# Optimization experiments

Hardware: AMD Instinct MI355X
Metric: run time of the kernel (lower is better)

Reference implementation:

```python
import jax, jax.numpy as jnp
import numpy as np

BN_EPS = 1e-5
C_IN, C_OUT, H, K = 16, 32, 300000, 27  # 3x3x3 kernel -> 27 taps


def setup_inputs() -> dict:
    key = jax.random.key(0)
    k1, k2, k3 = jax.random.split(key, 3)
    data_in = jax.random.normal(k1, (1, C_IN, H, 1), dtype=jnp.float32)
    weight = jax.random.normal(k2, (C_OUT, C_IN, K), dtype=jnp.float32) * 0.05
    gamma = jnp.ones((C_OUT,), dtype=jnp.float32)
    beta = jnp.zeros((C_OUT,), dtype=jnp.float32)
    neigh = jax.random.randint(k3, (H, K), 0, H, dtype=jnp.int64)
    return {"data_in": data_in, "weight": weight, "gamma": gamma,
            "beta": beta, "neigh": neigh}


def reference(data_in, weight, gamma, beta, neigh):
    # data_in: [1, C_in, H, 1] octree node features at a given depth
    x = data_in[0, :, :, 0]                       # [C_in, H]
    # octree2col: gather 27 neighbor taps per node; neigh<0 marks empty neighbors
    valid = neigh >= 0                            # [H, K]
    idx = jnp.where(valid, neigh, 0)
    col = x[:, idx] * valid[None].astype(x.dtype)  # [C_in, H, K]
    # conv as GEMM: weight [C_out, C_in, K]
    y = jnp.einsum('oik,ihk->oh', weight, col)     # [C_out, H]
    # BatchNorm2d (training mode): stats over N*H*W = node axis
    mean = jnp.mean(y, axis=1, keepdims=True)      # [C_out, 1]
    var = jnp.mean((y - mean) ** 2, axis=1, keepdims=True)
    y = (y - mean) * jax.lax.rsqrt(var + BN_EPS)
    y = y * gamma[:, None] + beta[:, None]
    return y[None, :, :, None]                     # [1, C_out, H, 1]
```

## Files before the change

### kernel.cpp

```cpp
#include <hip/hip_runtime.h>
#include <hip/hip_fp16.h>
#include <stdint.h>

static constexpr int CI = 16;
static constexpr int CO = 32;
static constexpr int H  = 300000;
static constexpr int K  = 27;
static constexpr float BN_EPS = 1e-5f;

typedef _Float16 h2_t __attribute__((ext_vector_type(2)));

__device__ __forceinline__ unsigned int pack_f16(float lo, float hi) {
    union { h2_t h; unsigned int u; } v;
    v.h[0] = (_Float16)lo;
    v.h[1] = (_Float16)hi;
    return v.u;
}

__device__ __forceinline__ float dot2f(unsigned int a, unsigned int b, float c) {
#if __has_builtin(__builtin_amdgcn_fdot2)
    union { unsigned int u; h2_t h; } ua, ub;
    ua.u = a; ub.u = b;
    return __builtin_amdgcn_fdot2(ua.h, ub.h, c, false);
#else
    union { unsigned int u; h2_t h; } ua, ub;
    ua.u = a; ub.u = b;
    float r = fmaf((float)ua.h[0], (float)ub.h[0], c);
    return fmaf((float)ua.h[1], (float)ub.h[1], r);
#endif
}

__global__ __launch_bounds__(256) void prep(const float* __restrict__ x,
                                            const float* __restrict__ w,
                                            unsigned int* __restrict__ xTp,
                                            unsigned int* __restrict__ wp,
                                            float* __restrict__ stats) {
    int h = blockIdx.x * 256 + threadIdx.x;
    if (h < H) {
        unsigned int r[8];
        #pragma unroll
        for (int j = 0; j < 8; ++j)
            r[j] = pack_f16(x[(size_t)(2 * j) * H + h], x[(size_t)(2 * j + 1) * H + h]);
        uint4* dst = reinterpret_cast<uint4*>(xTp + (size_t)h * 8);
        dst[0] = make_uint4(r[0], r[1], r[2], r[3]);
        dst[1] = make_uint4(r[4], r[5], r[6], r[7]);
    }
    if (blockIdx.x == 0) {
        for (int idx = threadIdx.x; idx < K * CO * 8; idx += 256) {
            int j = idx & 7;
            int o = (idx >> 3) & 31;
            int k = idx >> 8;
            float lo = w[((size_t)o * CI + 2 * j) * K + k];
            float hi = w[((size_t)o * CI + 2 * j + 1) * K + k];
            wp[idx] = pack_f16(lo, hi);
        }
        if (threadIdx.x < 64) stats[threadIdx.x] = 0.f;
    }
}

__global__ __launch_bounds__(256) void conv(const unsigned int* __restrict__ xTp,
                                            const unsigned int* __restrict__ wp,
                                            const int* __restrict__ neigh,
                                            float* __restrict__ out,
                                            float* __restrict__ stats) {
    __shared__ int snb[256 * K];
    const int t = threadIdx.x;
    const int h = blockIdx.x * 256 + t;

    {
        const int base = blockIdx.x * 256 * K;
        #pragma unroll 1
        for (int s = t; s < 256 * K; s += 256) {
            int g = base + s;
            snb[s] = (g < H * K) ? __builtin_nontemporal_load(&neigh[g]) : -1;
        }
    }
    __syncthreads();

    float acc[32];
    #pragma unroll
    for (int o = 0; o < 32; ++o) acc[o] = 0.f;

    if (h < H) {
        const int* np = &snb[t * K];

        int idx = np[0];
        const uint4* p0 = reinterpret_cast<const uint4*>(
            xTp + (size_t)(idx < 0 ? 0 : idx) * 8);
        uint4 a = p0[0];
        uint4 b = p0[1];

        for (int k = 0; k < K; ++k) {
            const int nidx = (k + 1 < K) ? np[k + 1] : 0;
            const uint4* p1 = reinterpret_cast<const uint4*>(
                xTp + (size_t)(nidx < 0 ? 0 : nidx) * 8);
            uint4 na = p1[0];
            uint4 nb = p1[1];

            if (idx < 0) {
                a.x = a.y = a.z = a.w = 0u;
                b.x = b.y = b.z = b.w = 0u;
            }

            const unsigned int* wk = wp + k * 256;
            #pragma unroll
            for (int o = 0; o < 32; ++o) {
                float s = acc[o];
                s = dot2f(a.x, wk[o * 8 + 0], s);
                s = dot2f(a.y, wk[o * 8 + 1], s);
                s = dot2f(a.z, wk[o * 8 + 2], s);
                s = dot2f(a.w, wk[o * 8 + 3], s);
                s = dot2f(b.x, wk[o * 8 + 4], s);
                s = dot2f(b.y, wk[o * 8 + 5], s);
                s = dot2f(b.z, wk[o * 8 + 6], s);
                s = dot2f(b.w, wk[o * 8 + 7], s);
                acc[o] = s;
            }

            idx = nidx; a = na; b = nb;
        }
        #pragma unroll
        for (int o = 0; o < 32; ++o)
            out[(size_t)o * H + h] = acc[o];
    }

    const unsigned lane = t & 63u;
    float mySum = 0.f, mySq = 0.f;
    #pragma unroll
    for (int o = 0; o < 32; ++o) {
        float v = acc[o];
        float q = v * v;
        #pragma unroll
        for (int d = 32; d > 0; d >>= 1) {
            v += __shfl_xor(v, d, 64);
            q += __shfl_xor(q, d, 64);
        }
        if (lane == (unsigned)o) { mySum = v; mySq = q; }
    }
    if (lane < 32u) {
        atomicAdd(&stats[lane], mySum);
        atomicAdd(&stats[32 + lane], mySq);
    }
}

__global__ __launch_bounds__(256) void bn_apply(float* __restrict__ out,
                                                const float* __restrict__ stats,
                                                const float* __restrict__ gamma,
                                                const float* __restrict__ beta) {
    size_t t = (size_t)blockIdx.x * 256 + threadIdx.x;
    size_t base = t * 4;
    if (base >= (size_t)CO * H) return;
    int o = (int)(base / (size_t)H);
    const float invH = 1.f / (float)H;
    float m   = stats[o] * invH;
    float var = stats[32 + o] * invH - m * m;
    float inv = rsqrtf(var + BN_EPS);
    float sc  = gamma[o] * inv;
    float sh  = beta[o] - m * sc;
    float4* p = reinterpret_cast<float4*>(out + base);
    float4 q = *p;
    q.x = q.x * sc + sh;
    q.y = q.y * sc + sh;
    q.z = q.z * sc + sh;
    q.w = q.w * sc + sh;
    *p = q;
}

extern "C" void kernel_launch(void* const* d_in, const int* in_sizes, int n_in,
                              void* d_out, int out_size, void* d_ws, size_t ws_size,
                              hipStream_t stream) {
    const float* x     = (const float*)d_in[0];
    const float* w     = (const float*)d_in[1];
    const float* gamma = (const float*)d_in[2];
    const float* beta  = (const float*)d_in[3];
    const int*   neigh = (const int*)d_in[4];
    float*       out   = (float*)d_out;

    char* ws = (char*)d_ws;
    const size_t XT_OFF    = 0;
    const size_t WP_OFF    = 9600000;
    const size_t STATS_OFF = 9627648;
    unsigned int* xTp   = (unsigned int*)(ws + XT_OFF);
    unsigned int* wp    = (unsigned int*)(ws + WP_OFF);
    float*        stats = (float*)(ws + STATS_OFF);

    const int HBP = (H + 255) / 256;
    prep<<<HBP, 256, 0, stream>>>(x, w, xTp, wp, stats);

    const int HBC = (H + 255) / 256;
    conv<<<HBC, 256, 0, stream>>>(xTp, wp, neigh, out, stats);

    const int NBN = (CO * H / 4 + 255) / 256;
    bn_apply<<<NBN, 256, 0, stream>>>(out, stats, gamma, beta);
}
```

Baseline: 346.6 us.

## Split the 27 kernel taps across two thread halves and combine in LDS

Each block now covers 128 nodes instead of 256, and the two halves of the block each process part of the 27 neighbor taps (14 and 13) for the same node. The partial 32-channel accumulators are combined through shared memory before the output store and the BN statistics reduction. This doubles the thread count per node to expose more parallelism and memory-level concurrency in the gather-bound conv. The cost is an extra LDS round trip, two barriers, and half the threads idling during the epilogue.

```diff
diff --git a/kernel.cpp b/kernel.cpp
--- a/kernel.cpp
+++ b/kernel.cpp
@@ -63,14 +63,18 @@
                                             const int* __restrict__ neigh,
                                             float* __restrict__ out,
                                             float* __restrict__ stats) {
-    __shared__ int snb[256 * K];
-    const int t = threadIdx.x;
-    const int h = blockIdx.x * 256 + t;
+    __shared__ float comb[128 * 36];
+    int* snb = reinterpret_cast<int*>(comb);
+
+    const int t  = threadIdx.x;
+    const int hl = t & 127;
+    const int kh = __builtin_amdgcn_readfirstlane(t >> 7);
+    const int h  = blockIdx.x * 128 + hl;
 
     {
-        const int base = blockIdx.x * 256 * K;
+        const int base = blockIdx.x * 128 * K;
         #pragma unroll 1
-        for (int s = t; s < 256 * K; s += 256) {
+        for (int s = t; s < 128 * K; s += 256) {
             int g = base + s;
             snb[s] = (g < H * K) ? __builtin_nontemporal_load(&neigh[g]) : -1;
         }
@@ -81,17 +85,20 @@
     #pragma unroll
     for (int o = 0; o < 32; ++o) acc[o] = 0.f;
 
+    const int k0   = kh * 14;
+    const int kend = 14 + kh * 13;
+
     if (h < H) {
-        const int* np = &snb[t * K];
-
-        int idx = np[0];
+        const int* np = &snb[hl * K];
+
+        int idx = np[k0];
         const uint4* p0 = reinterpret_cast<const uint4*>(
             xTp + (size_t)(idx < 0 ? 0 : idx) * 8);
         uint4 a = p0[0];
         uint4 b = p0[1];
 
-        for (int k = 0; k < K; ++k) {
-            const int nidx = (k + 1 < K) ? np[k + 1] : 0;
+        for (int k = k0; k < kend; ++k) {
+            const int nidx = (k + 1 < kend) ? np[k + 1] : 0;
             const uint4* p1 = reinterpret_cast<const uint4*>(
                 xTp + (size_t)(nidx < 0 ? 0 : nidx) * 8);
             uint4 na = p1[0];
@@ -119,27 +126,44 @@
 
             idx = nidx; a = na; b = nb;
         }
-        #pragma unroll
-        for (int o = 0; o < 32; ++o)
-            out[(size_t)o * H + h] = acc[o];
-    }
-
-    const unsigned lane = t & 63u;
-    float mySum = 0.f, mySq = 0.f;
-    #pragma unroll
-    for (int o = 0; o < 32; ++o) {
-        float v = acc[o];
-        float q = v * v;
-        #pragma unroll
-        for (int d = 32; d > 0; d >>= 1) {
-            v += __shfl_xor(v, d, 64);
-            q += __shfl_xor(q, d, 64);
-        }
-        if (lane == (unsigned)o) { mySum = v; mySq = q; }
-    }
-    if (lane < 32u) {
-        atomicAdd(&stats[lane], mySum);
-        atomicAdd(&stats[32 + lane], mySq);
+    }
+
+    __syncthreads();
+    if (kh == 1) {
+        float* c = &comb[hl * 36];
+        #pragma unroll
+        for (int o = 0; o < 32; ++o) c[o] = acc[o];
+    }
+    __syncthreads();
+
+    if (kh == 0) {
+        const float* c = &comb[hl * 36];
+        #pragma unroll
+        for (int o = 0; o < 32; ++o) acc[o] += c[o];
+
+        if (h < H) {
+            #pragma unroll
+            for (int o = 0; o < 32; ++o)
+                out[(size_t)o * H + h] = acc[o];
+        }
+
+        const unsigned lane = t & 63u;
+        float mySum = 0.f, mySq = 0.f;
+        #pragma unroll
+        for (int o = 0; o < 32; ++o) {
+            float v = acc[o];
+            float q = v * v;
+            #pragma unroll
+            for (int d = 32; d > 0; d >>= 1) {
+                v += __shfl_xor(v, d, 64);
+                q += __shfl_xor(q, d, 64);
+            }
+            if (lane == (unsigned)o) { mySum = v; mySq = q; }
+        }
+        if (lane < 32u) {
+            atomicAdd(&stats[lane], mySum);
+            atomicAdd(&stats[32 + lane], mySq);
+        }
     }
 }
 
@@ -187,7 +211,7 @@
     const int HBP = (H + 255) / 256;
     prep<<<HBP, 256, 0, stream>>>(x, w, xTp, wp, stats);
 
-    const int HBC = (H + 255) / 256;
+    const int HBC = (H + 127) / 128;
     conv<<<HBC, 256, 0, stream>>>(xTp, wp, neigh, out, stats);
 
     const int NBN = (CO * H / 4 + 255) / 256;
```

Result: slower. 428.4 us (+23.6%).
